# Kernel optimization log

Hardware: AMD Instinct MI355X
Metric: run time of the kernel (lower is better)

The kernel has to match this reference:

```python
import jax, jax.numpy as jnp
import numpy as np

CORR_WIDTH = 48
H_RADIUS = 3
V_RADIUS = 3


def _unfold_patches(img, vr, hr):
    # img: [b, c, h, w] -> [b, c*(2vr+1)*(2hr+1), h, w], zero-padded 'same'
    # (equivalent to nn.Unfold with padding=(hr, vr); channel ordering differs
    # from torch but the SSD reduction sums over all patch channels, so the
    # result is identical.)
    return jax.lax.conv_general_dilated_patches(
        img,
        filter_shape=(2 * vr + 1, 2 * hr + 1),
        window_strides=(1, 1),
        padding=((vr, vr), (hr, hr)),
    )


def setup_inputs() -> dict:
    key = jax.random.key(0)
    k1, k2 = jax.random.split(key)
    im_left = jax.random.normal(k1, (2, 16, 128, 256), dtype=jnp.float32)
    im_right = jax.random.normal(k2, (2, 16, 128, 256), dtype=jnp.float32)
    return {"im_left": im_left, "im_right": im_right}


def reference(im_left, im_right):
    cw, hr, vr = CORR_WIDTH, H_RADIUS, V_RADIUS
    b, c, h, w = im_left.shape
    # pad left image on the right edge by cw-1 zeros (ZeroPad2d((0, cw-1, 0, 0)))
    ext_l = jnp.pad(im_left, ((0, 0), (0, 0), (0, 0), (0, cw - 1)))
    patches_l = _unfold_patches(ext_l, vr, hr)    # [b, C, h, w+cw-1]
    patches_r = _unfold_patches(im_right, vr, hr)  # [b, C, h, w]

    # For each disparity d: cost[:, :, :, d] = sum_C (patches_l[..., d:d+w] - patches_r)^2
    # scan over disparities keeps peak memory at O(b*C*h*w) instead of
    # materializing the full [b, C, h, w, cw] broadcast difference.
    def step(carry, d):
        sl = jax.lax.dynamic_slice_in_dim(patches_l, d, w, axis=3)  # [b,C,h,w]
        cost_d = jnp.sum(jnp.square(sl - patches_r), axis=1)        # [b,h,w]
        return carry, cost_d

    _, cost = jax.lax.scan(step, None, jnp.arange(cw))  # [cw, b, h, w]
    return jnp.transpose(cost, (1, 2, 3, 0))            # [b, h, w, cw]
```

## Files before the change

kernel.cpp:

```cpp
#include <hip/hip_runtime.h>
#include <stdint.h>

#define CW 48
#define HR 3
#define VR 3
#define BB 2
#define CC 16
#define HH 128
#define WW 256

#define LW 312
#define RW2 264
#define SW 264
#define FWD (WW*CW)
#define HSEG 8

__device__ __forceinline__ uint32_t bf16rn(float f) {
    uint32_t x = __builtin_bit_cast(uint32_t, f);
    uint32_t lsb = (x >> 16) & 1u;
    x += 0x7fffu + lsb;
    return x >> 16;
}

__global__ __launch_bounds__(512) void ssd_hraw(
    const float* __restrict__ Lg, const float* __restrict__ Rg,
    uint16_t* __restrict__ Hws)
{
    const int bid = blockIdx.x;
    const int y   = bid % HH;
    const int b   = bid / HH;
    const int tid = threadIdx.x;

    __shared__ float Lsh[CC * LW];
    __shared__ float Rsh[CC * RW2];
    __shared__ float Ssh[CW * SW];
    __shared__ float el[LW];
    __shared__ float er[RW2];

    for (int i = tid; i < CC * 56; i += 512) {
        int c = i / 56, j = i % 56;
        int idx = (j < 3) ? j : (256 + j);
        Lsh[c * LW + idx] = 0.f;
    }
    for (int i = tid; i < CC * 8; i += 512) {
        int c = i >> 3, j = i & 7;
        int idx = (j < 3) ? j : (256 + j);
        Rsh[c * RW2 + idx] = 0.f;
    }
    if (tid < 56) { int idx = (tid < 3) ? tid : (256 + tid); el[idx] = 0.f; }
    else if (tid < 64) { int j = tid - 56; int idx = (j < 3) ? j : (256 + j); er[idx] = 0.f; }

    {
        const int img = tid >> 8;
        const int col = tid & 255;
        const float* __restrict__ base =
            (img ? Rg : Lg) + ((size_t)b * CC) * (HH * WW) + (size_t)y * WW + col;
        float* sh = (img ? &Rsh[HR + col] : &Lsh[HR + col]);
        const int stride = img ? RW2 : LW;
        float e = 0.f;
        #pragma unroll
        for (int c = 0; c < CC; ++c) {
            float v = base[(size_t)c * (HH * WW)];
            sh[c * stride] = v;
            e = fmaf(v, v, e);
        }
        (img ? er : el)[HR + col] = e;
    }
    __syncthreads();

    const int chalf = tid >> 8;
    const int unit  = tid & 255;
    const int q     = unit >> 6;
    const int xi0   = (unit & 63) * 4;
    const int d0    = q * 12;

    float acc[12][4];
    #pragma unroll
    for (int dd = 0; dd < 12; ++dd)
        #pragma unroll
        for (int xv = 0; xv < 4; ++xv) acc[dd][xv] = 0.f;

    {
        const int c0 = chalf * 8;
        #pragma unroll
        for (int ci = 0; ci < 8; ++ci) {
            const int c = c0 + ci;
            const float4 rv = *(const float4*)&Rsh[c * RW2 + xi0];
            const float rr[4] = {rv.x, rv.y, rv.z, rv.w};
            float lv[16];
            #pragma unroll
            for (int k = 0; k < 4; ++k)
                *(float4*)&lv[4 * k] = *(const float4*)&Lsh[c * LW + xi0 + d0 + 4 * k];
            #pragma unroll
            for (int dd = 0; dd < 12; ++dd)
                #pragma unroll
                for (int xv = 0; xv < 4; ++xv)
                    acc[dd][xv] = fmaf(lv[dd + xv], rr[xv], acc[dd][xv]);
        }
    }

    if (chalf == 0) {
        float elv[16];
        #pragma unroll
        for (int k = 0; k < 4; ++k)
            *(float4*)&elv[4 * k] = *(const float4*)&el[xi0 + d0 + 4 * k];
        const float4 e4 = *(const float4*)&er[xi0];
        const float err4[4] = {e4.x, e4.y, e4.z, e4.w};
        #pragma unroll
        for (int dd = 0; dd < 12; ++dd) {
            float4 o;
            o.x = elv[dd + 0] + err4[0] - 2.f * acc[dd][0];
            o.y = elv[dd + 1] + err4[1] - 2.f * acc[dd][1];
            o.z = elv[dd + 2] + err4[2] - 2.f * acc[dd][2];
            o.w = elv[dd + 3] + err4[3] - 2.f * acc[dd][3];
            *(float4*)&Ssh[(d0 + dd) * SW + xi0] = o;
        }
    } else {
        for (int p = tid - 256; p < 6 * CW; p += 256) {
            int dd = p % CW;
            int xi = 256 + p / CW;
            float a = 0.f;
            #pragma unroll
            for (int c = 0; c < CC; ++c)
                a = fmaf(Lsh[c * LW + xi + dd], Rsh[c * RW2 + xi], a);
            Ssh[dd * SW + xi] = el[xi + dd] + er[xi] - 2.f * a;
        }
    }
    __syncthreads();

    if (chalf == 1) {
        #pragma unroll
        for (int dd = 0; dd < 12; ++dd) {
            float4 v = *(const float4*)&Ssh[(d0 + dd) * SW + xi0];
            v.x = fmaf(-2.f, acc[dd][0], v.x);
            v.y = fmaf(-2.f, acc[dd][1], v.y);
            v.z = fmaf(-2.f, acc[dd][2], v.z);
            v.w = fmaf(-2.f, acc[dd][3], v.w);
            *(float4*)&Ssh[(d0 + dd) * SW + xi0] = v;
        }
    }
    __syncthreads();

    {
        const int j   = tid & 127;
        const int qh  = tid >> 7;
        const int w0  = 2 * j;
        const int dh0 = qh * 12;
        float hs[12][2];
        #pragma unroll
        for (int dd = 0; dd < 12; ++dd) {
            const float* row = &Ssh[(dh0 + dd) * SW + w0];
            const float2 r0 = *(const float2*)&row[0];
            const float2 r1 = *(const float2*)&row[2];
            const float2 r2 = *(const float2*)&row[4];
            const float2 r3 = *(const float2*)&row[6];
            float h0 = r0.x + r0.y + r1.x + r1.y + r2.x + r2.y + r3.x;
            hs[dd][0] = h0;
            hs[dd][1] = h0 - r0.x + r3.y;
        }
        uint16_t* H = Hws + (size_t)(b * HH + y) * FWD;
        #pragma unroll
        for (int xv = 0; xv < 2; ++xv) {
            uint32_t pk[6];
            #pragma unroll
            for (int i = 0; i < 6; ++i)
                pk[i] = bf16rn(hs[2 * i][xv]) | (bf16rn(hs[2 * i + 1][xv]) << 16);
            uint32_t* p = (uint32_t*)(H + (size_t)(w0 + xv) * CW + dh0);
            *(uint2*)&p[0] = make_uint2(pk[0], pk[1]);
            *(uint2*)&p[2] = make_uint2(pk[2], pk[3]);
            *(uint2*)&p[4] = make_uint2(pk[4], pk[5]);
        }
    }
}

__global__ __launch_bounds__(256) void vbox(
    const uint16_t* __restrict__ Hws, float* __restrict__ out)
{
    const int bid = blockIdx.x;
    const int g   = bid % 24;
    const int hs  = (bid / 24) % (HH / HSEG);
    const int b   = bid / (24 * (HH / HSEG));
    const int f2  = g * 256 + threadIdx.x;
    const int h0  = hs * HSEG;

    const uint16_t* H = Hws + (size_t)b * HH * FWD + 2 * f2;
    float*          O = out + (size_t)b * HH * FWD + 2 * f2;

    float vlo[HSEG + 6], vhi[HSEG + 6];
    if (h0 >= 3 && h0 + HSEG + 2 < HH) {
        #pragma unroll
        for (int k = 0; k < HSEG + 6; ++k) {
            uint32_t u = *(const uint32_t*)&H[(size_t)(h0 - 3 + k) * FWD];
            vlo[k] = __builtin_bit_cast(float, u << 16);
            vhi[k] = __builtin_bit_cast(float, u & 0xffff0000u);
        }
    } else {
        #pragma unroll
        for (int k = 0; k < HSEG + 6; ++k) {
            int yy = h0 - 3 + k;
            if (yy >= 0 && yy < HH) {
                uint32_t u = *(const uint32_t*)&H[(size_t)yy * FWD];
                vlo[k] = __builtin_bit_cast(float, u << 16);
                vhi[k] = __builtin_bit_cast(float, u & 0xffff0000u);
            } else { vlo[k] = 0.f; vhi[k] = 0.f; }
        }
    }
    #pragma unroll
    for (int hi = 0; hi < HSEG; ++hi) {
        float slo = vlo[hi], shi = vhi[hi];
        #pragma unroll
        for (int k = 1; k < 7; ++k) { slo += vlo[hi + k]; shi += vhi[hi + k]; }
        *(float2*)&O[(size_t)(h0 + hi) * FWD] = make_float2(slo, shi);
    }
}

extern "C" void kernel_launch(void* const* d_in, const int* in_sizes, int n_in,
                              void* d_out, int out_size, void* d_ws, size_t ws_size,
                              hipStream_t stream) {
    const float* L = (const float*)d_in[0];
    const float* R = (const float*)d_in[1];
    float* outp = (float*)d_out;
    uint16_t* Hws = (uint16_t*)d_ws;

    ssd_hraw<<<dim3(BB * HH), 512, 0, stream>>>(L, R, Hws);
    vbox<<<dim3(BB * (HH / HSEG) * 24), 256, 0, stream>>>(Hws, outp);
}
```

Before: 21.40 us.

## Store per-row SSD scratch as bf16 in LDS and widen vbox to 4 outputs

```diff
diff --git a/kernel.cpp b/kernel.cpp
--- a/kernel.cpp
+++ b/kernel.cpp
@@ -21,8 +21,14 @@
     x += 0x7fffu + lsb;
     return x >> 16;
 }
-
-__global__ __launch_bounds__(512) void ssd_hraw(
+__device__ __forceinline__ float bflo(uint32_t u) {
+    return __builtin_bit_cast(float, u << 16);
+}
+__device__ __forceinline__ float bfhi(uint32_t u) {
+    return __builtin_bit_cast(float, u & 0xffff0000u);
+}
+
+__global__ __launch_bounds__(512, 4) void ssd_hraw(
     const float* __restrict__ Lg, const float* __restrict__ Rg,
     uint16_t* __restrict__ Hws)
 {
@@ -31,11 +37,11 @@
     const int b   = bid / HH;
     const int tid = threadIdx.x;
 
-    __shared__ float Lsh[CC * LW];
-    __shared__ float Rsh[CC * RW2];
-    __shared__ float Ssh[CW * SW];
-    __shared__ float el[LW];
-    __shared__ float er[RW2];
+    __shared__ float    Lsh[CC * LW];
+    __shared__ float    Rsh[CC * RW2];
+    __shared__ uint16_t Sshb[CW * SW];
+    __shared__ float    el[LW];
+    __shared__ float    er[RW2];
 
     for (int i = tid; i < CC * 56; i += 512) {
         int c = i / 56, j = i % 56;
@@ -108,12 +114,13 @@
         const float err4[4] = {e4.x, e4.y, e4.z, e4.w};
         #pragma unroll
         for (int dd = 0; dd < 12; ++dd) {
-            float4 o;
-            o.x = elv[dd + 0] + err4[0] - 2.f * acc[dd][0];
-            o.y = elv[dd + 1] + err4[1] - 2.f * acc[dd][1];
-            o.z = elv[dd + 2] + err4[2] - 2.f * acc[dd][2];
-            o.w = elv[dd + 3] + err4[3] - 2.f * acc[dd][3];
-            *(float4*)&Ssh[(d0 + dd) * SW + xi0] = o;
+            float o0 = elv[dd + 0] + err4[0] - 2.f * acc[dd][0];
+            float o1 = elv[dd + 1] + err4[1] - 2.f * acc[dd][1];
+            float o2 = elv[dd + 2] + err4[2] - 2.f * acc[dd][2];
+            float o3 = elv[dd + 3] + err4[3] - 2.f * acc[dd][3];
+            uint2 pk = make_uint2(bf16rn(o0) | (bf16rn(o1) << 16),
+                                  bf16rn(o2) | (bf16rn(o3) << 16));
+            *(uint2*)&Sshb[(d0 + dd) * SW + xi0] = pk;
         }
     } else {
         for (int p = tid - 256; p < 6 * CW; p += 256) {
@@ -123,7 +130,7 @@
             #pragma unroll
             for (int c = 0; c < CC; ++c)
                 a = fmaf(Lsh[c * LW + xi + dd], Rsh[c * RW2 + xi], a);
-            Ssh[dd * SW + xi] = el[xi + dd] + er[xi] - 2.f * a;
+            Sshb[dd * SW + xi] = (uint16_t)bf16rn(el[xi + dd] + er[xi] - 2.f * a);
         }
     }
     __syncthreads();
@@ -131,12 +138,14 @@
     if (chalf == 1) {
         #pragma unroll
         for (int dd = 0; dd < 12; ++dd) {
-            float4 v = *(const float4*)&Ssh[(d0 + dd) * SW + xi0];
-            v.x = fmaf(-2.f, acc[dd][0], v.x);
-            v.y = fmaf(-2.f, acc[dd][1], v.y);
-            v.z = fmaf(-2.f, acc[dd][2], v.z);
-            v.w = fmaf(-2.f, acc[dd][3], v.w);
-            *(float4*)&Ssh[(d0 + dd) * SW + xi0] = v;
+            uint2 u = *(const uint2*)&Sshb[(d0 + dd) * SW + xi0];
+            float v0 = fmaf(-2.f, acc[dd][0], bflo(u.x));
+            float v1 = fmaf(-2.f, acc[dd][1], bfhi(u.x));
+            float v2 = fmaf(-2.f, acc[dd][2], bflo(u.y));
+            float v3 = fmaf(-2.f, acc[dd][3], bfhi(u.y));
+            *(uint2*)&Sshb[(d0 + dd) * SW + xi0] =
+                make_uint2(bf16rn(v0) | (bf16rn(v1) << 16),
+                           bf16rn(v2) | (bf16rn(v3) << 16));
         }
     }
     __syncthreads();
@@ -149,14 +158,13 @@
         float hs[12][2];
         #pragma unroll
         for (int dd = 0; dd < 12; ++dd) {
-            const float* row = &Ssh[(dh0 + dd) * SW + w0];
-            const float2 r0 = *(const float2*)&row[0];
-            const float2 r1 = *(const float2*)&row[2];
-            const float2 r2 = *(const float2*)&row[4];
-            const float2 r3 = *(const float2*)&row[6];
-            float h0 = r0.x + r0.y + r1.x + r1.y + r2.x + r2.y + r3.x;
+            const uint32_t* row = (const uint32_t*)&Sshb[(dh0 + dd) * SW + w0];
+            uint32_t u0 = row[0], u1 = row[1], u2 = row[2], u3 = row[3];
+            float x0 = bflo(u0), x1 = bfhi(u0), x2 = bflo(u1), x3 = bfhi(u1);
+            float x4 = bflo(u2), x5 = bfhi(u2), x6 = bflo(u3), x7 = bfhi(u3);
+            float h0 = x0 + x1 + x2 + x3 + x4 + x5 + x6;
             hs[dd][0] = h0;
-            hs[dd][1] = h0 - r0.x + r3.y;
+            hs[dd][1] = h0 - x0 + x7;
         }
         uint16_t* H = Hws + (size_t)(b * HH + y) * FWD;
         #pragma unroll
@@ -177,40 +185,46 @@
     const uint16_t* __restrict__ Hws, float* __restrict__ out)
 {
     const int bid = blockIdx.x;
-    const int g   = bid % 24;
-    const int hs  = (bid / 24) % (HH / HSEG);
-    const int b   = bid / (24 * (HH / HSEG));
-    const int f2  = g * 256 + threadIdx.x;
+    const int g   = bid % 12;
+    const int hs  = (bid / 12) % (HH / HSEG);
+    const int b   = bid / (12 * (HH / HSEG));
+    const int fb  = (g * 256 + threadIdx.x) * 4;
     const int h0  = hs * HSEG;
 
-    const uint16_t* H = Hws + (size_t)b * HH * FWD + 2 * f2;
-    float*          O = out + (size_t)b * HH * FWD + 2 * f2;
-
-    float vlo[HSEG + 6], vhi[HSEG + 6];
+    const uint16_t* H = Hws + (size_t)b * HH * FWD + fb;
+    float*          O = out + (size_t)b * HH * FWD + fb;
+
+    float v[HSEG + 6][4];
     if (h0 >= 3 && h0 + HSEG + 2 < HH) {
         #pragma unroll
         for (int k = 0; k < HSEG + 6; ++k) {
-            uint32_t u = *(const uint32_t*)&H[(size_t)(h0 - 3 + k) * FWD];
-            vlo[k] = __builtin_bit_cast(float, u << 16);
-            vhi[k] = __builtin_bit_cast(float, u & 0xffff0000u);
+            uint2 u = *(const uint2*)&H[(size_t)(h0 - 3 + k) * FWD];
+            v[k][0] = bflo(u.x); v[k][1] = bfhi(u.x);
+            v[k][2] = bflo(u.y); v[k][3] = bfhi(u.y);
         }
     } else {
         #pragma unroll
         for (int k = 0; k < HSEG + 6; ++k) {
             int yy = h0 - 3 + k;
             if (yy >= 0 && yy < HH) {
-                uint32_t u = *(const uint32_t*)&H[(size_t)yy * FWD];
-                vlo[k] = __builtin_bit_cast(float, u << 16);
-                vhi[k] = __builtin_bit_cast(float, u & 0xffff0000u);
-            } else { vlo[k] = 0.f; vhi[k] = 0.f; }
-        }
-    }
+                uint2 u = *(const uint2*)&H[(size_t)yy * FWD];
+                v[k][0] = bflo(u.x); v[k][1] = bfhi(u.x);
+                v[k][2] = bflo(u.y); v[k][3] = bfhi(u.y);
+            } else { v[k][0] = v[k][1] = v[k][2] = v[k][3] = 0.f; }
+        }
+    }
+
+    float s0 = 0.f, s1 = 0.f, s2 = 0.f, s3 = 0.f;
     #pragma unroll
-    for (int hi = 0; hi < HSEG; ++hi) {
-        float slo = vlo[hi], shi = vhi[hi];
-        #pragma unroll
-        for (int k = 1; k < 7; ++k) { slo += vlo[hi + k]; shi += vhi[hi + k]; }
-        *(float2*)&O[(size_t)(h0 + hi) * FWD] = make_float2(slo, shi);
+    for (int k = 0; k < 7; ++k) { s0 += v[k][0]; s1 += v[k][1]; s2 += v[k][2]; s3 += v[k][3]; }
+    *(float4*)&O[(size_t)h0 * FWD] = make_float4(s0, s1, s2, s3);
+    #pragma unroll
+    for (int hi = 1; hi < HSEG; ++hi) {
+        s0 += v[hi + 6][0] - v[hi - 1][0];
+        s1 += v[hi + 6][1] - v[hi - 1][1];
+        s2 += v[hi + 6][2] - v[hi - 1][2];
+        s3 += v[hi + 6][3] - v[hi - 1][3];
+        *(float4*)&O[(size_t)(h0 + hi) * FWD] = make_float4(s0, s1, s2, s3);
     }
 }
 
@@ -223,5 +237,5 @@
     uint16_t* Hws = (uint16_t*)d_ws;
 
     ssd_hraw<<<dim3(BB * HH), 512, 0, stream>>>(L, R, Hws);
-    vbox<<<dim3(BB * (HH / HSEG) * 24), 256, 0, stream>>>(Hws, outp);
-}
+    vbox<<<dim3(BB * (HH / HSEG) * 12), 256, 0, stream>>>(Hws, outp);
+}
```

Measured after the change: 24.22 us. 13.2% more time.
